# Optimization experiments

Measured on AMD Instinct MI355X. Metric: run time of the kernel, lower is better.

The kernel has to match this reference:

```python
import jax, jax.numpy as jnp
import numpy as np

LN2 = 0.6931471805599453

def _logcosh(z):
    # numerically stable log(cosh(z)) = logaddexp(z, -z) - log(2)
    return jnp.logaddexp(z, -z) - LN2

def _logpsi(z, W, b, a):
    # RBM log-amplitude. z: [..., N] -> scalar per leading dims
    return z @ a + jnp.sum(_logcosh(z @ W + b), axis=-1)

def setup_inputs() -> dict:
    key = jax.random.key(0)
    k0, k1, k2, k3, k4 = jax.random.split(key, 5)
    B, N, H = 64, 512, 2048
    # spin configurations (sign pattern; flips y_k = x with site k negated work for any real values)
    x = jnp.sign(jax.random.normal(k0, (B, N), dtype=jnp.float32))
    # small init so exp(logpsi_y - logpsi_x) stays well-scaled
    W = 0.01 * jax.random.normal(k1, (N, H), dtype=jnp.float32)
    b = 0.01 * jax.random.normal(k2, (H,), dtype=jnp.float32)
    a = 0.01 * jax.random.normal(k3, (N,), dtype=jnp.float32)
    # per-connection operator matrix elements O(x, y_k)
    Oxy = jax.random.normal(k4, (N,), dtype=jnp.float32)
    return {"x": x, "W": W, "b": b, "a": a, "Oxy": Oxy}

def reference(x, W, b, a, Oxy):
    # eval_local_operator, vmapped over a batch of configurations.
    # operator.conn(x): y[k] = x with spin k flipped, with matrix element Oxy[k].
    B, N = x.shape
    flip = 1.0 - 2.0 * jnp.eye(N, dtype=x.dtype)          # [K=N, N]
    y = x[:, None, :] * flip[None, :, :]                  # [B, K, N] connected states
    logpsi_x = _logpsi(x, W, b, a)                        # [B]
    logpsi_y = _logpsi(y, W, b, a)                        # [B, K]
    # Oxy @ exp(logpsi_y - logpsi_x) per sample
    return jnp.einsum('k,bk->b', Oxy, jnp.exp(logpsi_y - logpsi_x[:, None]))
```

## Files before the change

### kernel.cpp

```cpp
#include <hip/hip_runtime.h>
#include <hip/hip_bf16.h>
#include <math.h>

constexpr int NB = 64;
constexpr int NN = 512;
constexpr int NH = 2048;
constexpr float LN2 = 0.6931471805599453f;

constexpr size_t OFF_T2  = 0;
constexpr size_t OFF_LC  = OFF_T2  + (size_t)NN*NH;
constexpr size_t OFF_XT  = OFF_LC  + NN;
constexpr size_t OFF_TT  = OFF_XT  + (size_t)NN*NB;
constexpr size_t OFF_THP = OFF_TT  + (size_t)NH*NB;
constexpr size_t OFF_DS  = OFF_THP + (size_t)16*NB*NH;

__global__ __launch_bounds__(256) void k_pre(const float* __restrict__ W,
                                             const float* __restrict__ x,
                                             float* __restrict__ t2,
                                             float* __restrict__ LC,
                                             float* __restrict__ xt) {
    int bid = blockIdx.x, tid = threadIdx.x;
    if (bid < NN) {
        int k = bid;
        const float4* wr = (const float4*)(W + (size_t)k * NH);
        float4* tr = (float4*)(t2 + (size_t)k * NH);
        float4 w0 = wr[tid], w1 = wr[tid + 256];
        float in[8] = {w0.x, w0.y, w0.z, w0.w, w1.x, w1.y, w1.z, w1.w};
        float t[8], lsum = 0.f;
#pragma unroll
        for (int i = 0; i < 8; i++) {
            float y  = 2.0f * in[i];
            float ay = fabsf(y);
            float e  = __expf(-2.0f * ay);
            t[i] = copysignf((1.0f - e) / (1.0f + e), y);
            lsum += ay + __logf(1.0f + e) - LN2;
        }
        tr[tid]       = make_float4(t[0], t[1], t[2], t[3]);
        tr[tid + 256] = make_float4(t[4], t[5], t[6], t[7]);
        __shared__ float red[256];
        red[tid] = lsum; __syncthreads();
        for (int s = 128; s > 0; s >>= 1) {
            if (tid < s) red[tid] += red[tid + s];
            __syncthreads();
        }
        if (tid == 0) LC[k] = red[0];
    } else {
        int base = (bid - NN) * 4096;
#pragma unroll
        for (int i = 0; i < 16; i++) {
            int tIdx = base + i * 256 + tid;
            int b = tIdx & 63, n = tIdx >> 6;
            xt[tIdx] = x[(size_t)b * NN + n];
        }
    }
}

__global__ __launch_bounds__(256) void k_gemm(const float* __restrict__ W,
                                              const float* __restrict__ xt,
                                              float* __restrict__ thp) {
    int tid = threadIdx.x;
    int h  = blockIdx.x * 256 + tid;
    int bt = blockIdx.y;
    int nc = blockIdx.z;
    float acc[16];
#pragma unroll
    for (int j = 0; j < 16; j++) acc[j] = 0.f;
    const float* xp = xt + (size_t)nc * 32 * NB + bt * 16;
    const float* wp = W + (size_t)(nc * 32) * NH + h;
#pragma unroll 4
    for (int n = 0; n < 32; n++) {
        float w = wp[(size_t)n * NH];
#pragma unroll
        for (int j = 0; j < 16; j++) acc[j] = fmaf(xp[n * NB + j], w, acc[j]);
    }
    float* op = thp + (size_t)nc * NB * NH + (size_t)(bt * 16) * NH + h;
#pragma unroll
    for (int j = 0; j < 16; j++) op[(size_t)j * NH] = acc[j];
}

__global__ __launch_bounds__(256) void k_tanh(const float* __restrict__ thp,
                                              const float* __restrict__ bvec,
                                              float* __restrict__ Tt) {
    int g = blockIdx.x * 256 + threadIdx.x;
    int h = g & (NH - 1), b = g >> 11;
    float th = bvec[h];
#pragma unroll
    for (int nc = 0; nc < 16; nc++) th += thp[(size_t)nc * NB * NH + g];
    float ay = fabsf(th);
    float e  = __expf(-2.0f * ay);
    Tt[(size_t)h * NB + b] = copysignf((1.0f - e) / (1.0f + e), th);
}

__global__ __launch_bounds__(256) void k_main(const float* __restrict__ t2,
                                              const float* __restrict__ Tt,
                                              const float* __restrict__ xt,
                                              float* __restrict__ dsum) {
    __shared__ float Tl[256 * NB];
    int tid = threadIdx.x;
    int kt  = blockIdx.x;
    int hc  = blockIdx.y;
    const float4* src = (const float4*)(Tt + (size_t)hc * 256 * NB);
    float4* dst = (float4*)Tl;
#pragma unroll
    for (int i = 0; i < 16; i++) dst[tid + i * 256] = src[tid + i * 256];
    __syncthreads();

    int wave = tid >> 6, lane = tid & 63;
    int k0 = __builtin_amdgcn_readfirstlane(kt * 8 + wave * 2);
    float ms0 = -xt[(size_t)k0 * NB + lane];
    float ms1 = -xt[(size_t)(k0 + 1) * NB + lane];
    const float* r0 = t2 + (size_t)k0 * NH + hc * 256;
    const float* r1 = r0 + NH;

    float lp0 = 0.f, lp1 = 0.f;
    for (int h0 = 0; h0 < 256; h0 += 32) {
        float p0 = 1.f, p1 = 1.f;
#pragma unroll
        for (int hh = 0; hh < 32; hh++) {
            int h = h0 + hh;
            float T = Tl[h * NB + lane];
            p0 *= fmaf(r0[h] * T, ms0, 1.0f);
            p1 *= fmaf(r1[h] * T, ms1, 1.0f);
        }
        lp0 += __logf(p0);
        lp1 += __logf(p1);
    }
    dsum[(size_t)hc * NN * NB + (size_t)k0 * NB + lane]       = lp0;
    dsum[(size_t)hc * NN * NB + (size_t)(k0 + 1) * NB + lane] = lp1;
}

__global__ void k_out(const float* __restrict__ dsum, const float* __restrict__ LC,
                      const float* __restrict__ xt, const float* __restrict__ a,
                      const float* __restrict__ Oxy, float* __restrict__ out) {
    int b = blockIdx.x, tid = threadIdx.x;
    float sum = 0.f;
    for (int k = tid; k < NN; k += 256) {
        float d = LC[k] - 2.0f * xt[(size_t)k * NB + b] * a[k];
#pragma unroll
        for (int hc = 0; hc < 8; hc++) d += dsum[(size_t)hc * NN * NB + (size_t)k * NB + b];
        sum += Oxy[k] * __expf(d);
    }
    __shared__ float red[256];
    red[tid] = sum; __syncthreads();
    for (int st = 128; st > 0; st >>= 1) {
        if (tid < st) red[tid] += red[tid + st];
        __syncthreads();
    }
    if (tid == 0) out[b] = red[0];
}

extern "C" void kernel_launch(void* const* d_in, const int* in_sizes, int n_in,
                              void* d_out, int out_size, void* d_ws, size_t ws_size,
                              hipStream_t stream) {
    const float* x    = (const float*)d_in[0];
    const float* W    = (const float*)d_in[1];
    const float* bvec = (const float*)d_in[2];
    const float* a    = (const float*)d_in[3];
    const float* Oxy  = (const float*)d_in[4];
    float* out = (float*)d_out;

    float* ws   = (float*)d_ws;
    float* t2   = ws + OFF_T2;
    float* LC   = ws + OFF_LC;
    float* xt   = ws + OFF_XT;
    float* Tt   = ws + OFF_TT;
    float* thp  = ws + OFF_THP;
    float* dsum = ws + OFF_DS;

    k_pre<<<NN + 8, 256, 0, stream>>>(W, x, t2, LC, xt);
    k_gemm<<<dim3(NH / 256, NB / 16, 16), 256, 0, stream>>>(W, xt, thp);
    k_tanh<<<NB * NH / 256, 256, 0, stream>>>(thp, bvec, Tt);
    k_main<<<dim3(NN / 8, NH / 256), 256, 0, stream>>>(t2, Tt, xt, dsum);
    k_out<<<NB, 256, 0, stream>>>(dsum, LC, xt, a, Oxy, out);
}
```

Measured before the change: 94.11 us.

## Fuse all five stages into one cooperative kernel with grid-wide syncs

```diff
diff --git a/kernel.cpp b/kernel.cpp
--- a/kernel.cpp
+++ b/kernel.cpp
@@ -1,11 +1,15 @@
 #include <hip/hip_runtime.h>
+#include <hip/hip_cooperative_groups.h>
 #include <hip/hip_bf16.h>
 #include <math.h>
+
+namespace cg = cooperative_groups;
 
 constexpr int NB = 64;
 constexpr int NN = 512;
 constexpr int NH = 2048;
 constexpr float LN2 = 0.6931471805599453f;
+constexpr int GRID = 512;
 
 constexpr size_t OFF_T2  = 0;
 constexpr size_t OFF_LC  = OFF_T2  + (size_t)NN*NH;
@@ -14,13 +18,27 @@
 constexpr size_t OFF_THP = OFF_TT  + (size_t)NH*NB;
 constexpr size_t OFF_DS  = OFF_THP + (size_t)16*NB*NH;
 
-__global__ __launch_bounds__(256) void k_pre(const float* __restrict__ W,
-                                             const float* __restrict__ x,
-                                             float* __restrict__ t2,
-                                             float* __restrict__ LC,
-                                             float* __restrict__ xt) {
+__global__ __launch_bounds__(256, 2) void k_fused(const float* __restrict__ W,
+                                                  const float* __restrict__ x,
+                                                  const float* __restrict__ bvec,
+                                                  const float* __restrict__ a,
+                                                  const float* __restrict__ Oxy,
+                                                  float* __restrict__ out,
+                                                  float* __restrict__ ws) {
+    cg::grid_group grid = cg::this_grid();
+    __shared__ float Tl[128 * NB];
+    __shared__ float red[256];
+
+    float* t2   = ws + OFF_T2;
+    float* LC   = ws + OFF_LC;
+    float* xt   = ws + OFF_XT;
+    float* Tt   = ws + OFF_TT;
+    float* thp  = ws + OFF_THP;
+    float* dsum = ws + OFF_DS;
+
     int bid = blockIdx.x, tid = threadIdx.x;
-    if (bid < NN) {
+
+    {
         int k = bid;
         const float4* wr = (const float4*)(W + (size_t)k * NH);
         float4* tr = (float4*)(t2 + (size_t)k * NH);
@@ -37,139 +55,121 @@
         }
         tr[tid]       = make_float4(t[0], t[1], t[2], t[3]);
         tr[tid + 256] = make_float4(t[4], t[5], t[6], t[7]);
-        __shared__ float red[256];
         red[tid] = lsum; __syncthreads();
         for (int s = 128; s > 0; s >>= 1) {
             if (tid < s) red[tid] += red[tid + s];
             __syncthreads();
         }
         if (tid == 0) LC[k] = red[0];
-    } else {
-        int base = (bid - NN) * 4096;
+        int idx = bid * 256 + tid;
+        int b = idx & 63, n = idx >> 6;
+        xt[idx] = x[(size_t)b * NN + n];
+    }
+    grid.sync();
+
+    {
+        int nc = bid & 15;
+        int bt = (bid >> 4) & 3;
+        int ht = bid >> 6;
+        int h  = ht * 256 + tid;
+        float acc[16];
 #pragma unroll
-        for (int i = 0; i < 16; i++) {
-            int tIdx = base + i * 256 + tid;
-            int b = tIdx & 63, n = tIdx >> 6;
-            xt[tIdx] = x[(size_t)b * NN + n];
+        for (int j = 0; j < 16; j++) acc[j] = 0.f;
+        const float* xp = xt + (size_t)nc * 32 * NB + bt * 16;
+        const float* wp = W + (size_t)(nc * 32) * NH + h;
+#pragma unroll 4
+        for (int n = 0; n < 32; n++) {
+            float w = wp[(size_t)n * NH];
+#pragma unroll
+            for (int j = 0; j < 16; j++) acc[j] = fmaf(xp[n * NB + j], w, acc[j]);
         }
+        float* op = thp + (size_t)nc * NB * NH + (size_t)(bt * 16) * NH + h;
+#pragma unroll
+        for (int j = 0; j < 16; j++) op[(size_t)j * NH] = acc[j];
     }
-}
+    grid.sync();
 
-__global__ __launch_bounds__(256) void k_gemm(const float* __restrict__ W,
-                                              const float* __restrict__ xt,
-                                              float* __restrict__ thp) {
-    int tid = threadIdx.x;
-    int h  = blockIdx.x * 256 + tid;
-    int bt = blockIdx.y;
-    int nc = blockIdx.z;
-    float acc[16];
+    {
+        int g = bid * 256 + tid;
+        int b = g >> 11, h = g & (NH - 1);
+        float th = bvec[h];
 #pragma unroll
-    for (int j = 0; j < 16; j++) acc[j] = 0.f;
-    const float* xp = xt + (size_t)nc * 32 * NB + bt * 16;
-    const float* wp = W + (size_t)(nc * 32) * NH + h;
-#pragma unroll 4
-    for (int n = 0; n < 32; n++) {
-        float w = wp[(size_t)n * NH];
+        for (int nc = 0; nc < 16; nc++) th += thp[(size_t)nc * NB * NH + g];
+        float ay = fabsf(th);
+        float e  = __expf(-2.0f * ay);
+        Tt[(size_t)h * NB + b] = copysignf((1.0f - e) / (1.0f + e), th);
+    }
+    grid.sync();
+
+    {
+        int hc = bid & 15;
+        int kt = bid >> 4;
+        const float4* src = (const float4*)(Tt + (size_t)hc * 128 * NB);
+        float4* dst = (float4*)Tl;
 #pragma unroll
-        for (int j = 0; j < 16; j++) acc[j] = fmaf(xp[n * NB + j], w, acc[j]);
+        for (int i = 0; i < 8; i++) dst[tid + i * 256] = src[tid + i * 256];
+        __syncthreads();
+
+        int wv = tid >> 6, lane = tid & 63;
+        int kb = __builtin_amdgcn_readfirstlane(kt * 16 + wv * 4);
+        float ms[4];
+        const float* rr[4];
+#pragma unroll
+        for (int j = 0; j < 4; j++) {
+            ms[j] = -xt[(size_t)(kb + j) * NB + lane];
+            rr[j] = t2 + (size_t)(kb + j) * NH + hc * 128;
+        }
+        float lp[4] = {0.f, 0.f, 0.f, 0.f};
+        for (int h0 = 0; h0 < 128; h0 += 32) {
+            float p[4] = {1.f, 1.f, 1.f, 1.f};
+#pragma unroll
+            for (int hh = 0; hh < 32; hh++) {
+                int h = h0 + hh;
+                float T = Tl[h * NB + lane];
+#pragma unroll
+                for (int j = 0; j < 4; j++)
+                    p[j] *= fmaf(rr[j][h] * T, ms[j], 1.0f);
+            }
+#pragma unroll
+            for (int j = 0; j < 4; j++) lp[j] += __logf(p[j]);
+        }
+#pragma unroll
+        for (int j = 0; j < 4; j++)
+            dsum[(size_t)hc * NN * NB + (size_t)(kb + j) * NB + lane] = lp[j];
     }
-    float* op = thp + (size_t)nc * NB * NH + (size_t)(bt * 16) * NH + h;
+    grid.sync();
+
+    if (bid < NB) {
+        int b = bid;
+        float sum = 0.f;
+        for (int k = tid; k < NN; k += 256) {
+            float d = LC[k] - 2.0f * xt[(size_t)k * NB + b] * a[k];
 #pragma unroll
-    for (int j = 0; j < 16; j++) op[(size_t)j * NH] = acc[j];
-}
-
-__global__ __launch_bounds__(256) void k_tanh(const float* __restrict__ thp,
-                                              const float* __restrict__ bvec,
-                                              float* __restrict__ Tt) {
-    int g = blockIdx.x * 256 + threadIdx.x;
-    int h = g & (NH - 1), b = g >> 11;
-    float th = bvec[h];
-#pragma unroll
-    for (int nc = 0; nc < 16; nc++) th += thp[(size_t)nc * NB * NH + g];
-    float ay = fabsf(th);
-    float e  = __expf(-2.0f * ay);
-    Tt[(size_t)h * NB + b] = copysignf((1.0f - e) / (1.0f + e), th);
-}
-
-__global__ __launch_bounds__(256) void k_main(const float* __restrict__ t2,
-                                              const float* __restrict__ Tt,
-                                              const float* __restrict__ xt,
-                                              float* __restrict__ dsum) {
-    __shared__ float Tl[256 * NB];
-    int tid = threadIdx.x;
-    int kt  = blockIdx.x;
-    int hc  = blockIdx.y;
-    const float4* src = (const float4*)(Tt + (size_t)hc * 256 * NB);
-    float4* dst = (float4*)Tl;
-#pragma unroll
-    for (int i = 0; i < 16; i++) dst[tid + i * 256] = src[tid + i * 256];
-    __syncthreads();
-
-    int wave = tid >> 6, lane = tid & 63;
-    int k0 = __builtin_amdgcn_readfirstlane(kt * 8 + wave * 2);
-    float ms0 = -xt[(size_t)k0 * NB + lane];
-    float ms1 = -xt[(size_t)(k0 + 1) * NB + lane];
-    const float* r0 = t2 + (size_t)k0 * NH + hc * 256;
-    const float* r1 = r0 + NH;
-
-    float lp0 = 0.f, lp1 = 0.f;
-    for (int h0 = 0; h0 < 256; h0 += 32) {
-        float p0 = 1.f, p1 = 1.f;
-#pragma unroll
-        for (int hh = 0; hh < 32; hh++) {
-            int h = h0 + hh;
-            float T = Tl[h * NB + lane];
-            p0 *= fmaf(r0[h] * T, ms0, 1.0f);
-            p1 *= fmaf(r1[h] * T, ms1, 1.0f);
+            for (int hc = 0; hc < 16; hc++)
+                d += dsum[(size_t)hc * NN * NB + (size_t)k * NB + b];
+            sum += Oxy[k] * __expf(d);
         }
-        lp0 += __logf(p0);
-        lp1 += __logf(p1);
+        red[tid] = sum; __syncthreads();
+        for (int s = 128; s > 0; s >>= 1) {
+            if (tid < s) red[tid] += red[tid + s];
+            __syncthreads();
+        }
+        if (tid == 0) out[b] = red[0];
     }
-    dsum[(size_t)hc * NN * NB + (size_t)k0 * NB + lane]       = lp0;
-    dsum[(size_t)hc * NN * NB + (size_t)(k0 + 1) * NB + lane] = lp1;
-}
-
-__global__ void k_out(const float* __restrict__ dsum, const float* __restrict__ LC,
-                      const float* __restrict__ xt, const float* __restrict__ a,
-                      const float* __restrict__ Oxy, float* __restrict__ out) {
-    int b = blockIdx.x, tid = threadIdx.x;
-    float sum = 0.f;
-    for (int k = tid; k < NN; k += 256) {
-        float d = LC[k] - 2.0f * xt[(size_t)k * NB + b] * a[k];
-#pragma unroll
-        for (int hc = 0; hc < 8; hc++) d += dsum[(size_t)hc * NN * NB + (size_t)k * NB + b];
-        sum += Oxy[k] * __expf(d);
-    }
-    __shared__ float red[256];
-    red[tid] = sum; __syncthreads();
-    for (int st = 128; st > 0; st >>= 1) {
-        if (tid < st) red[tid] += red[tid + st];
-        __syncthreads();
-    }
-    if (tid == 0) out[b] = red[0];
 }
 
 extern "C" void kernel_launch(void* const* d_in, const int* in_sizes, int n_in,
                               void* d_out, int out_size, void* d_ws, size_t ws_size,
                               hipStream_t stream) {
+    const float* W    = (const float*)d_in[1];
     const float* x    = (const float*)d_in[0];
-    const float* W    = (const float*)d_in[1];
     const float* bvec = (const float*)d_in[2];
     const float* a    = (const float*)d_in[3];
     const float* Oxy  = (const float*)d_in[4];
     float* out = (float*)d_out;
+    float* ws  = (float*)d_ws;
 
-    float* ws   = (float*)d_ws;
-    float* t2   = ws + OFF_T2;
-    float* LC   = ws + OFF_LC;
-    float* xt   = ws + OFF_XT;
-    float* Tt   = ws + OFF_TT;
-    float* thp  = ws + OFF_THP;
-    float* dsum = ws + OFF_DS;
-
-    k_pre<<<NN + 8, 256, 0, stream>>>(W, x, t2, LC, xt);
-    k_gemm<<<dim3(NH / 256, NB / 16, 16), 256, 0, stream>>>(W, xt, thp);
-    k_tanh<<<NB * NH / 256, 256, 0, stream>>>(thp, bvec, Tt);
-    k_main<<<dim3(NN / 8, NH / 256), 256, 0, stream>>>(t2, Tt, xt, dsum);
-    k_out<<<NB, 256, 0, stream>>>(dsum, LC, xt, a, Oxy, out);
+    void* args[] = {(void*)&W, (void*)&x, (void*)&bvec, (void*)&a,
+                    (void*)&Oxy, (void*)&out, (void*)&ws};
+    hipLaunchCooperativeKernel((void*)k_fused, dim3(GRID), dim3(256), args, 0, stream);
 }
```

New measurement: 351.0 us. 273% more time.
